# Optimization experiments

Hardware: AMD Instinct MI355X
Metric: run time of the kernel (lower is better)

## Reference

```python
import jax, jax.numpy as jnp
import numpy as np

EPS = 1e-3  # matches MaskedBatchNorm2d default eps=0.001


def setup_inputs() -> dict:
    key = jax.random.key(0)
    k1, k2 = jax.random.split(key)
    B, C, W, H = 16, 64, 256, 256
    x = jax.random.normal(k1, (B, C, W, H), dtype=jnp.float32)
    # densified sparse-voxel feature maps the module is designed for.
    keep = (jax.random.uniform(k2, (B, W, H)) < 0.3).astype(jnp.float32)
    x = x * keep[:, None, :, :]
    return {"x": x}


def reference(x):
    """Faithful masked batchnorm (training mode, affine=False).

    Original: per-batch nonzero() of channel-sum, pad index lists to the max
    count with zeros (i.e. duplicate location (0,0)), gather [B, Nmax, C],
    compute per-channel mean/var over ALL gathered entries (padding included),
    divide by sqrt(var+eps) (mean NOT subtracted in output), scatter back to
    nonzero locations — padded rows also overwrite location (0,0).
    """
    B, C, W, H = x.shape
    x1 = x.sum(axis=1)                      # [B, W, H]
    m = x1 != 0                             # nonzero-site mask
    mf = m.astype(x.dtype)
    n = mf.sum(axis=(1, 2))                 # nonzero count per batch item [B]
    Nmax = n.max()
    pad = Nmax - n                          # number of padded (0,0) duplicates per item
    total = (B * Nmax).astype(x.dtype)      # B * max(num_nonzeros)

    x00 = x[:, :, 0, 0]                     # [B, C] value gathered by padded indices

    # per-channel mean over masked sites + padded duplicates of (0,0)
    sum_c = jnp.einsum('bcwh,bwh->c', x, mf) + jnp.einsum('bc,b->c', x00, pad)
    mean = sum_c / total                    # [C]

    d = x - mean[None, :, None, None]
    var = (jnp.einsum('bcwh,bwh->c', d * d, mf)
           + jnp.einsum('bc,b->c', (x00 - mean[None, :]) ** 2, pad)) / total

    inv = 1.0 / jnp.sqrt(var + EPS)         # [C]; note: mean is NOT subtracted
    xn = x * inv[None, :, None, None]

    out = jnp.where(m[:, None, :, :], xn, x)
    # padded scatter rows write normalized x[b,:,0,0] into location (0,0)
    has_pad = (pad > 0)[:, None]            # [B,1]
    out = out.at[:, :, 0, 0].set(jnp.where(has_pad, x00 * inv[None, :], out[:, :, 0, 0]))
    return out
```

## Files before the change

### kernel.cpp

```cpp
#include <hip/hip_runtime.h>


#define NB 16
#define CB 64
#define WH 65536
#define TILE 256
#define NTILES (NB * WH / TILE)
#define GRID1 1024
#define TPT (NTILES / GRID1)
#define DIRTY_CAP 512
#define EPS 0.001f

typedef float f32x4 __attribute__((ext_vector_type(4)));


__global__ __launch_bounds__(512, 8)
void mbn_pass1(const float* __restrict__ x, float* __restrict__ sqPart,
               unsigned* __restrict__ nPart, unsigned* __restrict__ dirtyCnt,
               int* __restrict__ dirtyLoc) {
    __shared__ float lds_s[8][TILE];
    __shared__ float lds_a[8][TILE];
    __shared__ unsigned cnt_lds[16];
    const int tid  = threadIdx.x;
    const int wave = tid >> 6;
    const int lane = tid & 63;
    if (tid < 16) cnt_lds[tid] = 0;

    float sAcc[8], qAcc[8];
#pragma unroll
    for (int j = 0; j < 8; ++j) { sAcc[j] = 0.f; qAcc[j] = 0.f; }
    __syncthreads();

    for (int tt = 0; tt < TPT; ++tt) {
        const int tile = blockIdx.x + tt * GRID1;
        const int b    = tile >> 8;
        const int whb  = (tile & 255) * TILE;
        const float* base = x + (((size_t)(b * 64 + wave * 8)) << 16) + whb + lane * 4;

        float sp0 = 0.f, sp1 = 0.f, sp2 = 0.f, sp3 = 0.f;
        float aa0 = 0.f, aa1 = 0.f, aa2 = 0.f, aa3 = 0.f;
#pragma unroll
        for (int j = 0; j < 8; ++j) {
            float4 v = *(const float4*)(base + ((size_t)j << 16));
            sp0 += v.x; sp1 += v.y; sp2 += v.z; sp3 += v.w;
            aa0 += fabsf(v.x); aa1 += fabsf(v.y); aa2 += fabsf(v.z); aa3 += fabsf(v.w);
            sAcc[j] += (v.x + v.y) + (v.z + v.w);
            qAcc[j] = fmaf(v.x, v.x, qAcc[j]);
            qAcc[j] = fmaf(v.y, v.y, qAcc[j]);
            qAcc[j] = fmaf(v.z, v.z, qAcc[j]);
            qAcc[j] = fmaf(v.w, v.w, qAcc[j]);
        }
        *(float4*)&lds_s[wave][lane * 4] = make_float4(sp0, sp1, sp2, sp3);
        *(float4*)&lds_a[wave][lane * 4] = make_float4(aa0, aa1, aa2, aa3);
        __syncthreads();

        if (tid < TILE) {
            float s = lds_s[0][tid] + lds_s[1][tid] + lds_s[2][tid] + lds_s[3][tid]
                    + lds_s[4][tid] + lds_s[5][tid] + lds_s[6][tid] + lds_s[7][tid];
            float a = lds_a[0][tid] + lds_a[1][tid] + lds_a[2][tid] + lds_a[3][tid]
                    + lds_a[4][tid] + lds_a[5][tid] + lds_a[6][tid] + lds_a[7][tid];
            bool mask = (s != 0.0f);
            unsigned long long bal = __ballot(mask);
            if (lane == 0) atomicAdd(&cnt_lds[b], (unsigned)__popcll(bal));
            if (!mask && a != 0.0f) {
                unsigned idx = atomicAdd(dirtyCnt, 1u);
                if (idx < DIRTY_CAP) dirtyLoc[idx] = (b << 16) | (whb + tid);
            }
        }
        __syncthreads();
    }

#pragma unroll
    for (int j = 0; j < 8; ++j) {
        float sv = sAcc[j], qv = qAcc[j];
        for (int off = 32; off; off >>= 1) {
            sv += __shfl_xor(sv, off);
            qv += __shfl_xor(qv, off);
        }
        if (lane == 0) {
            sqPart[blockIdx.x * 128 + wave * 8 + j]      = sv;
            sqPart[blockIdx.x * 128 + 64 + wave * 8 + j] = qv;
        }
    }
    if (tid < 16) nPart[blockIdx.x * 16 + tid] = cnt_lds[tid];
}

__global__ __launch_bounds__(1024)
void mbn_finalize(const float* __restrict__ x, const float* __restrict__ sqPart,
                  const unsigned* __restrict__ nPart,
                  const unsigned* __restrict__ dirtyCnt, const int* __restrict__ dirtyLoc,
                  float* __restrict__ inv, int* __restrict__ padOut) {
    __shared__ float red[1024];
    __shared__ float sq[128];
    __shared__ unsigned npar[16][16];
    __shared__ unsigned ntot[16];
    const int t = threadIdx.x;
    const int col = t & 127, grp = t >> 7;

    float acc = 0.f;
    const float* p = sqPart + (size_t)grp * 128 * 128 + col;
#pragma unroll 8
    for (int r = 0; r < 128; ++r) acc += p[(size_t)r * 128];
    red[t] = acc;

    if (t < 256) {
        const int b = t & 15, g2 = t >> 4;
        unsigned s = 0;
        const unsigned* np = nPart + g2 * 64 * 16 + b;
#pragma unroll 8
        for (int r = 0; r < 64; ++r) s += np[r * 16];
        npar[g2][b] = s;
    }
    __syncthreads();
    if (t < 128) {
        float v = 0.f;
#pragma unroll
        for (int g2 = 0; g2 < 8; ++g2) v += red[g2 * 128 + t];
        sq[t] = v;
    }
    if (t < 16) {
        unsigned v = 0;
#pragma unroll
        for (int g2 = 0; g2 < 16; ++g2) v += npar[g2][t];
        ntot[t] = v;
    }
    __syncthreads();

    if (t < 64) {
        const int c = t;
        unsigned nmax = 0;
#pragma unroll
        for (int b = 0; b < NB; ++b) { unsigned nb = ntot[b]; nmax = nb > nmax ? nb : nmax; }
        const float total = (float)(16u * nmax);

        float s = sq[c], q = sq[64 + c];
        unsigned cnt = *dirtyCnt; if (cnt > DIRTY_CAP) cnt = DIRTY_CAP;
        for (unsigned i = 0; i < cnt; ++i) {
            int loc = dirtyLoc[i];
            int b = loc >> 16, wh = loc & 65535;
            float v = x[(((size_t)(b * 64 + c)) << 16) + wh];
            s -= v; q -= v * v;
        }
        float p1 = 0.f, p2 = 0.f;
#pragma unroll
        for (int b = 0; b < NB; ++b) {
            float padf = (float)(nmax - ntot[b]);
            float v00  = x[((size_t)(b * 64 + c)) << 16];
            p1 = fmaf(padf, v00, p1);
            p2 = fmaf(padf, v00 * v00, p2);
            if (c == 0) padOut[b] = (int)(nmax - ntot[b]);
        }
        float mean = (s + p1) / total;
        float var  = (q + p2) / total - mean * mean;
        inv[c] = 1.0f / sqrtf(var + EPS);
    }
}

__global__ __launch_bounds__(256)
void mbn_pass2(const float* __restrict__ x, float* __restrict__ out,
               const float* __restrict__ inv, const unsigned* __restrict__ dirtyCnt,
               const int* __restrict__ dirtyLoc, const int* __restrict__ padArr) {
    const int blk = blockIdx.x;
    const float sc = inv[(blk >> 3) & 63];
    const f32x4* x4 = (const f32x4*)x;
    f32x4* out4 = (f32x4*)out;
    const size_t base = (size_t)blk * 2048 + threadIdx.x;
#pragma unroll
    for (int k = 0; k < 8; ++k) {
        size_t i = base + (size_t)k * 256;
        f32x4 v = x4[i];
        v *= sc;
        __builtin_nontemporal_store(v, &out4[i]);
    }

    unsigned cnt = *dirtyCnt;
    if (cnt != 0) {
        __syncthreads();
        if (threadIdx.x == 0) {
            if (cnt > DIRTY_CAP) cnt = DIRTY_CAP;
            const int bb = blk >> 9, cc = (blk >> 3) & 63, seg = blk & 7;
            const int lo = seg * 8192, hi = lo + 8192;
            for (unsigned i = 0; i < cnt; ++i) {
                int loc = dirtyLoc[i];
                int b = loc >> 16, wh = loc & 65535;
                if (b != bb || wh < lo || wh >= hi) continue;
                if (wh == 0 && padArr[b] > 0) continue;
                size_t idx = (((size_t)(b * 64 + cc)) << 16) + wh;
                out[idx] = x[idx];
            }
        }
    }
}

extern "C" void kernel_launch(void* const* d_in, const int* in_sizes, int n_in,
                              void* d_out, int out_size, void* d_ws, size_t ws_size,
                              hipStream_t stream) {
    const float* x = (const float*)d_in[0];
    float* out = (float*)d_out;
    float* wsf = (float*)d_ws;

    float*    sqPart   = wsf;
    unsigned* nPart    = (unsigned*)(wsf + 131072);
    unsigned* dirtyCnt = (unsigned*)(wsf + 147456);
    float*    inv      = wsf + 147520;
    int*      padArr   = (int*)(wsf + 147584);
    int*      dirtyLoc = (int*)(wsf + 147600);

    hipMemsetAsync((char*)d_ws + 147456 * 4, 0, 64, stream);

    mbn_pass1<<<GRID1, 512, 0, stream>>>(x, sqPart, nPart, dirtyCnt, dirtyLoc);
    mbn_finalize<<<1, 1024, 0, stream>>>(x, sqPart, nPart, dirtyCnt, dirtyLoc, inv, padArr);
    mbn_pass2<<<8192, 256, 0, stream>>>(x, out, inv, dirtyCnt, dirtyLoc, padArr);
}
```

Measured before the change: 564.1 us.

## Give each pass1 block one contiguous strip and reduce site sums with LDS atomics

Each pass1 block now handles one contiguous 1024-site strip of a single batch item instead of looping over interleaved 256-site tiles. That removes the per-tile barrier pairs and the staged 8-way cross-wave LDS reduction. Per-site channel sums are gathered with LDS float atomicAdd, and the nonzero check uses an atomicOr of absolute-value bit patterns instead of summing fabs. The cost is many LDS atomics per element, 8 waves contending on the same addresses, and a channel-sum order that changes between runs.

Measured after the change: 782.8 us. 38.8% more time.

```diff
diff --git a/kernel.cpp b/kernel.cpp
--- a/kernel.cpp
+++ b/kernel.cpp
@@ -4,10 +4,8 @@
 #define NB 16
 #define CB 64
 #define WH 65536
-#define TILE 256
-#define NTILES (NB * WH / TILE)
+#define STRIP 1024
 #define GRID1 1024
-#define TPT (NTILES / GRID1)
 #define DIRTY_CAP 512
 #define EPS 0.001f
 
@@ -18,57 +16,65 @@
 void mbn_pass1(const float* __restrict__ x, float* __restrict__ sqPart,
                unsigned* __restrict__ nPart, unsigned* __restrict__ dirtyCnt,
                int* __restrict__ dirtyLoc) {
-    __shared__ float lds_s[8][TILE];
-    __shared__ float lds_a[8][TILE];
-    __shared__ unsigned cnt_lds[16];
+    __shared__ float    lds_sum[STRIP];
+    __shared__ unsigned lds_or[STRIP];
+    __shared__ unsigned cnt_lds;
     const int tid  = threadIdx.x;
     const int wave = tid >> 6;
     const int lane = tid & 63;
-    if (tid < 16) cnt_lds[tid] = 0;
+    const int b    = blockIdx.x >> 6;
+    const int whb  = (blockIdx.x & 63) * STRIP;
+
+    for (int i = tid; i < STRIP; i += 512) { lds_sum[i] = 0.f; lds_or[i] = 0u; }
+    if (tid == 0) cnt_lds = 0u;
+    __syncthreads();
 
     float sAcc[8], qAcc[8];
 #pragma unroll
     for (int j = 0; j < 8; ++j) { sAcc[j] = 0.f; qAcc[j] = 0.f; }
-    __syncthreads();
-
-    for (int tt = 0; tt < TPT; ++tt) {
-        const int tile = blockIdx.x + tt * GRID1;
-        const int b    = tile >> 8;
-        const int whb  = (tile & 255) * TILE;
-        const float* base = x + (((size_t)(b * 64 + wave * 8)) << 16) + whb + lane * 4;
-
-        float sp0 = 0.f, sp1 = 0.f, sp2 = 0.f, sp3 = 0.f;
-        float aa0 = 0.f, aa1 = 0.f, aa2 = 0.f, aa3 = 0.f;
-#pragma unroll
-        for (int j = 0; j < 8; ++j) {
-            float4 v = *(const float4*)(base + ((size_t)j << 16));
-            sp0 += v.x; sp1 += v.y; sp2 += v.z; sp3 += v.w;
-            aa0 += fabsf(v.x); aa1 += fabsf(v.y); aa2 += fabsf(v.z); aa3 += fabsf(v.w);
+
+    const float* xb = x + (((size_t)(b * 64 + wave * 8)) << 16) + whb;
+#pragma unroll
+    for (int j = 0; j < 8; ++j) {
+        const float* p = xb + ((size_t)j << 16);
+#pragma unroll
+        for (int k = 0; k < 4; ++k) {
+            const int l = k * 256 + lane * 4;
+            float4 v = *(const float4*)(p + l);
             sAcc[j] += (v.x + v.y) + (v.z + v.w);
             qAcc[j] = fmaf(v.x, v.x, qAcc[j]);
             qAcc[j] = fmaf(v.y, v.y, qAcc[j]);
             qAcc[j] = fmaf(v.z, v.z, qAcc[j]);
             qAcc[j] = fmaf(v.w, v.w, qAcc[j]);
-        }
-        *(float4*)&lds_s[wave][lane * 4] = make_float4(sp0, sp1, sp2, sp3);
-        *(float4*)&lds_a[wave][lane * 4] = make_float4(aa0, aa1, aa2, aa3);
-        __syncthreads();
-
-        if (tid < TILE) {
-            float s = lds_s[0][tid] + lds_s[1][tid] + lds_s[2][tid] + lds_s[3][tid]
-                    + lds_s[4][tid] + lds_s[5][tid] + lds_s[6][tid] + lds_s[7][tid];
-            float a = lds_a[0][tid] + lds_a[1][tid] + lds_a[2][tid] + lds_a[3][tid]
-                    + lds_a[4][tid] + lds_a[5][tid] + lds_a[6][tid] + lds_a[7][tid];
-            bool mask = (s != 0.0f);
-            unsigned long long bal = __ballot(mask);
-            if (lane == 0) atomicAdd(&cnt_lds[b], (unsigned)__popcll(bal));
-            if (!mask && a != 0.0f) {
-                unsigned idx = atomicAdd(dirtyCnt, 1u);
-                if (idx < DIRTY_CAP) dirtyLoc[idx] = (b << 16) | (whb + tid);
-            }
-        }
-        __syncthreads();
-    }
+            const int si = (l >> 2);
+            atomicAdd(&lds_sum[si], v.x);
+            atomicAdd(&lds_sum[256 + si], v.y);
+            atomicAdd(&lds_sum[512 + si], v.z);
+            atomicAdd(&lds_sum[768 + si], v.w);
+            atomicOr(&lds_or[si],       __float_as_uint(v.x) & 0x7fffffffu);
+            atomicOr(&lds_or[256 + si], __float_as_uint(v.y) & 0x7fffffffu);
+            atomicOr(&lds_or[512 + si], __float_as_uint(v.z) & 0x7fffffffu);
+            atomicOr(&lds_or[768 + si], __float_as_uint(v.w) & 0x7fffffffu);
+        }
+    }
+    __syncthreads();
+
+    unsigned cnt = 0;
+#pragma unroll
+    for (int h = 0; h < 2; ++h) {
+        const int idx = tid + h * 512;
+        const float    s = lds_sum[idx];
+        const unsigned o = lds_or[idx];
+        const bool kept = (s != 0.0f);
+        cnt += kept ? 1u : 0u;
+        if (!kept && o != 0u) {
+            const int l = ((idx & 255) << 2) | (idx >> 8);
+            unsigned di = atomicAdd(dirtyCnt, 1u);
+            if (di < DIRTY_CAP) dirtyLoc[di] = (b << 16) | (whb + l);
+        }
+    }
+    for (int off = 32; off; off >>= 1) cnt += __shfl_xor(cnt, off);
+    if (lane == 0) atomicAdd(&cnt_lds, cnt);
 
 #pragma unroll
     for (int j = 0; j < 8; ++j) {
@@ -82,7 +88,8 @@
             sqPart[blockIdx.x * 128 + 64 + wave * 8 + j] = qv;
         }
     }
-    if (tid < 16) nPart[blockIdx.x * 16 + tid] = cnt_lds[tid];
+    __syncthreads();
+    if (tid < 16) nPart[blockIdx.x * 16 + tid] = (tid == b) ? cnt_lds : 0u;
 }
 
 __global__ __launch_bounds__(1024)
```

## Fuse finalize into pass1 via last-block ticket and defer per-tile reductions

Applied to the files above, without the earlier changes.

Removes the separate single-block finalize launch: each pass1 block takes an atomic ticket, and the last block to finish reduces the partials and computes inv and pad counts. The per-tile mask reduction is now deferred, so all TPT tiles are staged in LDS first and the two barriers per tile collapse into one. The abs-sum used for dirty detection is replaced by a bitwise OR of magnitudes through LDS atomics. This saves a launch gap and in-loop barriers, at the cost of more LDS per block (which may lower occupancy) and a serial tail on the last block.

Measured after the change: 888.2 us. 57.5% more time.

```diff
diff --git a/kernel.cpp b/kernel.cpp
--- a/kernel.cpp
+++ b/kernel.cpp
@@ -17,20 +17,26 @@
 __global__ __launch_bounds__(512, 8)
 void mbn_pass1(const float* __restrict__ x, float* __restrict__ sqPart,
                unsigned* __restrict__ nPart, unsigned* __restrict__ dirtyCnt,
-               int* __restrict__ dirtyLoc) {
-    __shared__ float lds_s[8][TILE];
-    __shared__ float lds_a[8][TILE];
+               int* __restrict__ dirtyLoc, float* __restrict__ inv,
+               int* __restrict__ padArr, unsigned* __restrict__ ticket) {
+    __shared__ float    lds_s[TPT][8][TILE];
+    __shared__ unsigned lds_or[TPT][TILE];
     __shared__ unsigned cnt_lds[16];
+    __shared__ unsigned lastFlag;
     const int tid  = threadIdx.x;
     const int wave = tid >> 6;
     const int lane = tid & 63;
+
+    for (int i = tid; i < TPT * TILE; i += 512) ((unsigned*)lds_or)[i] = 0u;
     if (tid < 16) cnt_lds[tid] = 0;
+    if (tid == 0) lastFlag = 0;
 
     float sAcc[8], qAcc[8];
 #pragma unroll
     for (int j = 0; j < 8; ++j) { sAcc[j] = 0.f; qAcc[j] = 0.f; }
     __syncthreads();
 
+#pragma unroll
     for (int tt = 0; tt < TPT; ++tt) {
         const int tile = blockIdx.x + tt * GRID1;
         const int b    = tile >> 8;
@@ -38,36 +44,46 @@
         const float* base = x + (((size_t)(b * 64 + wave * 8)) << 16) + whb + lane * 4;
 
         float sp0 = 0.f, sp1 = 0.f, sp2 = 0.f, sp3 = 0.f;
-        float aa0 = 0.f, aa1 = 0.f, aa2 = 0.f, aa3 = 0.f;
+        unsigned o0 = 0u, o1 = 0u, o2 = 0u, o3 = 0u;
 #pragma unroll
         for (int j = 0; j < 8; ++j) {
             float4 v = *(const float4*)(base + ((size_t)j << 16));
             sp0 += v.x; sp1 += v.y; sp2 += v.z; sp3 += v.w;
-            aa0 += fabsf(v.x); aa1 += fabsf(v.y); aa2 += fabsf(v.z); aa3 += fabsf(v.w);
+            o0 |= __float_as_uint(v.x) & 0x7fffffffu;
+            o1 |= __float_as_uint(v.y) & 0x7fffffffu;
+            o2 |= __float_as_uint(v.z) & 0x7fffffffu;
+            o3 |= __float_as_uint(v.w) & 0x7fffffffu;
             sAcc[j] += (v.x + v.y) + (v.z + v.w);
             qAcc[j] = fmaf(v.x, v.x, qAcc[j]);
             qAcc[j] = fmaf(v.y, v.y, qAcc[j]);
             qAcc[j] = fmaf(v.z, v.z, qAcc[j]);
             qAcc[j] = fmaf(v.w, v.w, qAcc[j]);
         }
-        *(float4*)&lds_s[wave][lane * 4] = make_float4(sp0, sp1, sp2, sp3);
-        *(float4*)&lds_a[wave][lane * 4] = make_float4(aa0, aa1, aa2, aa3);
-        __syncthreads();
-
-        if (tid < TILE) {
-            float s = lds_s[0][tid] + lds_s[1][tid] + lds_s[2][tid] + lds_s[3][tid]
-                    + lds_s[4][tid] + lds_s[5][tid] + lds_s[6][tid] + lds_s[7][tid];
-            float a = lds_a[0][tid] + lds_a[1][tid] + lds_a[2][tid] + lds_a[3][tid]
-                    + lds_a[4][tid] + lds_a[5][tid] + lds_a[6][tid] + lds_a[7][tid];
-            bool mask = (s != 0.0f);
-            unsigned long long bal = __ballot(mask);
-            if (lane == 0) atomicAdd(&cnt_lds[b], (unsigned)__popcll(bal));
-            if (!mask && a != 0.0f) {
-                unsigned idx = atomicAdd(dirtyCnt, 1u);
-                if (idx < DIRTY_CAP) dirtyLoc[idx] = (b << 16) | (whb + tid);
-            }
-        }
-        __syncthreads();
+        *(float4*)&lds_s[tt][wave][lane * 4] = make_float4(sp0, sp1, sp2, sp3);
+        if (o0) atomicOr(&lds_or[tt][lane * 4 + 0], o0);
+        if (o1) atomicOr(&lds_or[tt][lane * 4 + 1], o1);
+        if (o2) atomicOr(&lds_or[tt][lane * 4 + 2], o2);
+        if (o3) atomicOr(&lds_or[tt][lane * 4 + 3], o3);
+    }
+    __syncthreads();
+
+#pragma unroll
+    for (int h = 0; h < 2; ++h) {
+        const int pi  = tid + h * 512;
+        const int tt  = pi >> 8, loc = pi & 255;
+        const int tile = blockIdx.x + tt * GRID1;
+        const int b    = tile >> 8;
+        float s = ((lds_s[tt][0][loc] + lds_s[tt][1][loc])
+                 + (lds_s[tt][2][loc] + lds_s[tt][3][loc]))
+                + ((lds_s[tt][4][loc] + lds_s[tt][5][loc])
+                 + (lds_s[tt][6][loc] + lds_s[tt][7][loc]));
+        bool kept = (s != 0.0f);
+        unsigned long long bal = __ballot(kept);
+        if (lane == 0) atomicAdd(&cnt_lds[b], (unsigned)__popcll(bal));
+        if (!kept && lds_or[tt][loc] != 0u) {
+            unsigned di = atomicAdd(dirtyCnt, 1u);
+            if (di < DIRTY_CAP) dirtyLoc[di] = (b << 16) | ((tile & 255) * TILE + loc);
+        }
     }
 
 #pragma unroll
@@ -82,52 +98,52 @@
             sqPart[blockIdx.x * 128 + 64 + wave * 8 + j] = qv;
         }
     }
+    __syncthreads();
     if (tid < 16) nPart[blockIdx.x * 16 + tid] = cnt_lds[tid];
-}
-
-__global__ __launch_bounds__(1024)
-void mbn_finalize(const float* __restrict__ x, const float* __restrict__ sqPart,
-                  const unsigned* __restrict__ nPart,
-                  const unsigned* __restrict__ dirtyCnt, const int* __restrict__ dirtyLoc,
-                  float* __restrict__ inv, int* __restrict__ padOut) {
-    __shared__ float red[1024];
-    __shared__ float sq[128];
-    __shared__ unsigned npar[16][16];
-    __shared__ unsigned ntot[16];
-    const int t = threadIdx.x;
-    const int col = t & 127, grp = t >> 7;
-
-    float acc = 0.f;
-    const float* p = sqPart + (size_t)grp * 128 * 128 + col;
+
+    __threadfence();
+    __syncthreads();
+    if (tid == 0) {
+        unsigned t = atomicAdd(ticket, 1u);
+        if (t == GRID1 - 1) lastFlag = 1u;
+    }
+    __syncthreads();
+    if (!lastFlag) return;
+
+    __threadfence();
+    float*    red  = (float*)&lds_s[0][0][0];
+    float*    sq   = red + 512;
+    unsigned* npar = (unsigned*)(sq + 128);
+    unsigned* ntot = npar + 256;
+
+    const int col = tid & 127, grp = tid >> 7;
+    {
+        float acc = 0.f;
+        const float* p = sqPart + (size_t)grp * 256 * 128 + col;
 #pragma unroll 8
-    for (int r = 0; r < 128; ++r) acc += p[(size_t)r * 128];
-    red[t] = acc;
-
-    if (t < 256) {
-        const int b = t & 15, g2 = t >> 4;
+        for (int r = 0; r < 256; ++r) acc += p[(size_t)r * 128];
+        red[tid] = acc;
+    }
+    if (tid < 256) {
+        const int b = tid & 15, g2 = tid >> 4;
         unsigned s = 0;
         const unsigned* np = nPart + g2 * 64 * 16 + b;
 #pragma unroll 8
         for (int r = 0; r < 64; ++r) s += np[r * 16];
-        npar[g2][b] = s;
-    }
-    __syncthreads();
-    if (t < 128) {
-        float v = 0.f;
-#pragma unroll
-        for (int g2 = 0; g2 < 8; ++g2) v += red[g2 * 128 + t];
-        sq[t] = v;
-    }
-    if (t < 16) {
+        npar[g2 * 16 + b] = s;
+    }
+    __syncthreads();
+    if (tid < 128) sq[tid] = (red[tid] + red[128 + tid]) + (red[256 + tid] + red[384 + tid]);
+    if (tid < 16) {
         unsigned v = 0;
 #pragma unroll
-        for (int g2 = 0; g2 < 16; ++g2) v += npar[g2][t];
-        ntot[t] = v;
-    }
-    __syncthreads();
-
-    if (t < 64) {
-        const int c = t;
+        for (int g2 = 0; g2 < 16; ++g2) v += npar[g2 * 16 + tid];
+        ntot[tid] = v;
+    }
+    __syncthreads();
+
+    if (tid < 64) {
+        const int c = tid;
         unsigned nmax = 0;
 #pragma unroll
         for (int b = 0; b < NB; ++b) { unsigned nb = ntot[b]; nmax = nb > nmax ? nb : nmax; }
@@ -148,7 +164,7 @@
             float v00  = x[((size_t)(b * 64 + c)) << 16];
             p1 = fmaf(padf, v00, p1);
             p2 = fmaf(padf, v00 * v00, p2);
-            if (c == 0) padOut[b] = (int)(nmax - ntot[b]);
+            if (c == 0) padArr[b] = (int)(nmax - ntot[b]);
         }
         float mean = (s + p1) / total;
         float var  = (q + p2) / total - mean * mean;
@@ -202,13 +218,14 @@
     float*    sqPart   = wsf;
     unsigned* nPart    = (unsigned*)(wsf + 131072);
     unsigned* dirtyCnt = (unsigned*)(wsf + 147456);
+    unsigned* ticket   = dirtyCnt + 1;
     float*    inv      = wsf + 147520;
     int*      padArr   = (int*)(wsf + 147584);
     int*      dirtyLoc = (int*)(wsf + 147600);
 
     hipMemsetAsync((char*)d_ws + 147456 * 4, 0, 64, stream);
 
-    mbn_pass1<<<GRID1, 512, 0, stream>>>(x, sqPart, nPart, dirtyCnt, dirtyLoc);
-    mbn_finalize<<<1, 1024, 0, stream>>>(x, sqPart, nPart, dirtyCnt, dirtyLoc, inv, padArr);
+    mbn_pass1<<<GRID1, 512, 0, stream>>>(x, sqPart, nPart, dirtyCnt, dirtyLoc,
+                                         inv, padArr, ticket);
     mbn_pass2<<<8192, 256, 0, stream>>>(x, out, inv, dirtyCnt, dirtyLoc, padArr);
 }
```
